# Kernel tuning notes

Measured on AMD Instinct MI355X. Metric: run time of the kernel, lower is better.

Reference implementation:

```python
import jax, jax.numpy as jnp
import numpy as np

N_FFT = 256
FS = 256.0
FREQ_BINS = [(0.0, 4.0), (4.0, 8.0), (8.0, 13.0), (13.0, 30.0),
             (30.0, 45.0), (45.0, 70.0), (70.0, 100.0), (100.0, 128.0)]


def _build_freq_masks():
    # rfftfreq for n_fft=256, d=1/fs -> 129 bins at 1 Hz spacing
    freqs_hz = np.fft.rfftfreq(N_FFT, d=1.0 / FS)
    masks = np.stack([(freqs_hz > lo) & (freqs_hz <= hi) for lo, hi in FREQ_BINS])
    assert (masks.sum(axis=1) > 0).all(), 'each band must contain at least one FFT bin'
    return jnp.asarray(masks, dtype=jnp.float32)  # (band=8, freq=129)


def setup_inputs() -> dict:
    key = jax.random.key(0)
    x = jax.random.normal(key, (8, 50, 129, 32, 32), dtype=jnp.float32)
    freq_masks = _build_freq_masks()  # (8, 129)
    return {'x': x, 'freq_masks': freq_masks}


def reference(x, freq_masks):
    # Equivalent to broadcast (b t 1 f c1 c2) * (1 1 g f 1 1) then sum over f,
    # expressed as a contraction so the blown-up intermediate is never built.
    # x: (b, t, f, c1, c2); freq_masks: (g, f) -> out: (b, t, g, c1, c2)
    band_sums = jnp.einsum('btfij,gf->btgij', x, freq_masks)
    counts = freq_masks.sum(axis=1)  # (g,)
    return band_sums / counts[None, None, :, None, None]
```

## Files before the change

kernel.cpp:

```cpp
#include <hip/hip_runtime.h>


#define BT   400
#define NF   129
#define NG   8
#define NC   1024

__global__ __launch_bounds__(256)
void band_avg_kernel(const float* __restrict__ x,
                     const float* __restrict__ masks,
                     float* __restrict__ out)
{
    const int blk = blockIdx.x;
    const int bt  = blk >> 3;
    const int g   = blk & 7;
    const int tid = threadIdx.x;

    __shared__ int   s_start, s_end;
    __shared__ float s_cnt, s_inv;
    if (tid == 0) { s_start = NF; s_end = -1; s_cnt = 0.0f; }
    __syncthreads();
    if (tid < NF) {
        float m = masks[g * NF + tid];
        if (m > 0.0f) {
            atomicMin(&s_start, tid);
            atomicMax(&s_end, tid);
            atomicAdd(&s_cnt, m);
        }
    }
    __syncthreads();
    if (tid == 0) s_inv = 1.0f / s_cnt;
    __syncthreads();

    const int   f0  = s_start;
    const int   f1  = s_end;
    const float inv = s_inv;

    const float4* xin = reinterpret_cast<const float4*>(
                            x + (size_t)bt * NF * NC) + tid;
    float4 acc = make_float4(0.0f, 0.0f, 0.0f, 0.0f);
    for (int f = f0; f <= f1; ++f) {
        float4 v = xin[(size_t)f * (NC / 4)];
        acc.x += v.x; acc.y += v.y; acc.z += v.z; acc.w += v.w;
    }
    acc.x *= inv; acc.y *= inv; acc.z *= inv; acc.w *= inv;

    float4* o = reinterpret_cast<float4*>(
                    out + ((size_t)bt * NG + g) * NC) + tid;
    *o = acc;
}

extern "C" void kernel_launch(void* const* d_in, const int* in_sizes, int n_in,
                              void* d_out, int out_size, void* d_ws, size_t ws_size,
                              hipStream_t stream) {
    const float* x     = (const float*)d_in[0];
    const float* masks = (const float*)d_in[1];
    float*       out   = (float*)d_out;
    band_avg_kernel<<<dim3(BT * NG), dim3(256), 0, stream>>>(x, masks, out);
}
```

Before: 305.4 us.

## Scan masks per thread, reorder blocks by band, unroll accumulation by two

Each thread now scans the 129 mask values itself, replacing the shared-memory atomics and three barriers that found each band's range and count. Blocks are now ordered band-major, so consecutive blocks read the same frequency range of adjacent (b,t) slices. The frequency accumulation uses two independent vector accumulators to keep two loads in flight. The per-thread 129-iteration mask scan adds redundant scalar/L1 loads per thread, and the band-major order changes how concurrently running blocks share cached x rows.

```diff
diff --git a/kernel.cpp b/kernel.cpp
--- a/kernel.cpp
+++ b/kernel.cpp
@@ -6,47 +6,47 @@
 #define NG   8
 #define NC   1024
 
+typedef float v4f __attribute__((ext_vector_type(4)));
+
 __global__ __launch_bounds__(256)
-void band_avg_kernel(const float* __restrict__ x,
-                     const float* __restrict__ masks,
-                     float* __restrict__ out)
+void band_avg_v2(const float* __restrict__ x,
+                 const float* __restrict__ masks,
+                 float* __restrict__ out)
 {
     const int blk = blockIdx.x;
-    const int bt  = blk >> 3;
-    const int g   = blk & 7;
+    const int bt  = blk % BT;
+    const int g   = blk / BT;
     const int tid = threadIdx.x;
 
-    __shared__ int   s_start, s_end;
-    __shared__ float s_cnt, s_inv;
-    if (tid == 0) { s_start = NF; s_end = -1; s_cnt = 0.0f; }
-    __syncthreads();
-    if (tid < NF) {
-        float m = masks[g * NF + tid];
+    int f0 = -1, f1 = -1;
+    float cnt = 0.0f;
+    for (int f = 0; f < NF; ++f) {
+        float m = masks[g * NF + f];
         if (m > 0.0f) {
-            atomicMin(&s_start, tid);
-            atomicMax(&s_end, tid);
-            atomicAdd(&s_cnt, m);
+            if (f0 < 0) f0 = f;
+            f1 = f;
+            cnt += m;
         }
     }
-    __syncthreads();
-    if (tid == 0) s_inv = 1.0f / s_cnt;
-    __syncthreads();
+    const float inv = 1.0f / cnt;
 
-    const int   f0  = s_start;
-    const int   f1  = s_end;
-    const float inv = s_inv;
+    const v4f* xin = reinterpret_cast<const v4f*>(x + (size_t)bt * NF * NC) + tid;
 
-    const float4* xin = reinterpret_cast<const float4*>(
-                            x + (size_t)bt * NF * NC) + tid;
-    float4 acc = make_float4(0.0f, 0.0f, 0.0f, 0.0f);
-    for (int f = f0; f <= f1; ++f) {
-        float4 v = xin[(size_t)f * (NC / 4)];
-        acc.x += v.x; acc.y += v.y; acc.z += v.z; acc.w += v.w;
+    v4f a0 = {0.0f, 0.0f, 0.0f, 0.0f};
+    v4f a1 = {0.0f, 0.0f, 0.0f, 0.0f};
+    int f = f0;
+    for (; f + 1 <= f1; f += 2) {
+        v4f u = xin[(size_t)f       * (NC / 4)];
+        v4f w = xin[(size_t)(f + 1) * (NC / 4)];
+        a0 += u;
+        a1 += w;
     }
-    acc.x *= inv; acc.y *= inv; acc.z *= inv; acc.w *= inv;
+    if (f <= f1) {
+        a0 += xin[(size_t)f * (NC / 4)];
+    }
+    v4f acc = (a0 + a1) * inv;
 
-    float4* o = reinterpret_cast<float4*>(
-                    out + ((size_t)bt * NG + g) * NC) + tid;
+    v4f* o = reinterpret_cast<v4f*>(out + ((size_t)bt * NG + g) * NC) + tid;
     *o = acc;
 }
 
@@ -56,5 +56,5 @@
     const float* x     = (const float*)d_in[0];
     const float* masks = (const float*)d_in[1];
     float*       out   = (float*)d_out;
-    band_avg_kernel<<<dim3(BT * NG), dim3(256), 0, stream>>>(x, masks, out);
+    band_avg_v2<<<dim3(BT * NG), dim3(256), 0, stream>>>(x, masks, out);
 }
```

After: 304.7 us. No clear change (-0.2%).
